# Kernel optimization log

Hardware: AMD Instinct MI355X
Metric: run time of the kernel (lower is better)

## Reference

```python
import jax, jax.numpy as jnp
import numpy as np

N_HEAD = 16
N_KV = 4
ROT = 128  # rotary_dim == head_dim
BASE = 10000
N_CTX = 1024


def make_sincos(n_ctx, rotary_dim, base):
    # GPT-NeoX style (rotary_adjacent_pairs=False): freq repeated twice
    pos = jnp.arange(n_ctx, dtype=jnp.float32)
    dim = jnp.arange(rotary_dim // 2, dtype=jnp.float32)
    freq = jnp.float32(base) ** (dim / (rotary_dim / 2))
    freq = jnp.tile(freq, 2)  # [rotary_dim]
    angles = pos[:, None] / freq[None, :]  # [n_ctx, rotary_dim]
    return jnp.sin(angles), jnp.cos(angles)


def setup_inputs() -> dict:
    key = jax.random.key(0)
    ks = jax.random.split(key, 5)
    B, T, C = 8, 1024, 2048
    r = N_HEAD // N_KV
    Ckv = C // r
    s = 0.02
    x = jax.random.normal(ks[0], (B, T, C), jnp.float32)
    wq = jax.random.normal(ks[1], (C, C), jnp.float32) * s
    wk = jax.random.normal(ks[2], (C, Ckv), jnp.float32) * s
    wv = jax.random.normal(ks[3], (C, Ckv), jnp.float32) * s
    wo = jax.random.normal(ks[4], (C, C), jnp.float32) * s
    sin, cos = make_sincos(N_CTX, ROT, BASE)
    return dict(x=x, wq=wq, wk=wk, wv=wv, wo=wo, sin=sin, cos=cos)


def _rope(x, sin, cos):
    # x: [B, H, T, hd]; rotary applied to first ROT dims (here ROT == hd)
    T = x.shape[2]
    n = ROT // 2
    x_rot = x[..., :ROT]
    x_pass = x[..., ROT:]
    # rotate_every_two (NeoX style): [x0..x_{n-1}, x_n..] -> [-x_n.., x0..]
    x_flip = jnp.concatenate([-x_rot[..., n:], x_rot[..., :n]], axis=-1)
    c = cos[None, None, :T, :]
    s = sin[None, None, :T, :]
    x_rotated = x_rot * c + x_flip * s
    return jnp.concatenate([x_rotated, x_pass], axis=-1)


def reference(x, wq, wk, wv, wo, sin, cos):
    B, T, C = x.shape
    H = N_HEAD
    hd = C // H
    r = H // N_KV
    q = (x @ wq).reshape(B, T, H, hd).transpose(0, 2, 1, 3)  # [B,H,T,hd]
    # Original: repeat_interleave along seq dim then view(B,T,H,hd).
    # Equivalent to tiling the kv channel vector r times per position.
    k = jnp.tile(x @ wk, (1, 1, r)).reshape(B, T, H, hd).transpose(0, 2, 1, 3)
    v = jnp.tile(x @ wv, (1, 1, r)).reshape(B, T, H, hd).transpose(0, 2, 1, 3)
    q = _rope(q, sin, cos)
    k = _rope(k, sin, cos)
    att = jnp.einsum('bhqd,bhkd->bhqk', q, k) / jnp.sqrt(jnp.float32(hd))
    causal = jnp.tril(jnp.ones((T, T), dtype=bool))
    att = jnp.where(causal[None, None], att, -jnp.inf)
    att = jax.nn.softmax(att, axis=-1)
    y = jnp.einsum('bhqk,bhkd->bhqd', att, v)
    y = y.transpose(0, 2, 1, 3).reshape(B, T, C)
    return y @ wo
```

## Files before the change

kernel.cpp:

```cpp
#include <hip/hip_runtime.h>

typedef __attribute__((ext_vector_type(8))) short short8;
typedef __attribute__((ext_vector_type(4))) float f32x4;

#define B_    8
#define T_    1024
#define C_    2048
#define H_    16
#define HKV_  4
#define HD_   128
#define M_    8192
#define NQKV_ 3072
#define KDIM_ 2048

__device__ __forceinline__ unsigned short f2bf(float f) {
  unsigned u = __float_as_uint(f);
  u += 0x7FFF + ((u >> 16) & 1);
  return (unsigned short)(u >> 16);
}
__device__ __forceinline__ float bf2f(unsigned short h) {
  return __uint_as_float(((unsigned)h) << 16);
}

__device__ __forceinline__ void async16(const unsigned short* g, unsigned short* l) {
  __builtin_amdgcn_global_load_lds(
      (const unsigned int __attribute__((address_space(1)))*)g,
      (unsigned int __attribute__((address_space(3)))*)l,
      16, 0, 0);
}

__global__ __launch_bounds__(256) void cvt_bf16_kernel(const float* __restrict__ in,
                                                       unsigned short* __restrict__ out) {
  int idx = blockIdx.x * 256 + threadIdx.x;
  float4 v = ((const float4*)in)[idx];
  ushort4 o;
  o.x = f2bf(v.x); o.y = f2bf(v.y); o.z = f2bf(v.z); o.w = f2bf(v.w);
  ((ushort4*)out)[idx] = o;
}

__global__ __launch_bounds__(256) void tpose_f32_bf16(const float* __restrict__ in,
                                                      unsigned short* __restrict__ out,
                                                      int Cc, int ldo) {
  __shared__ unsigned short tile[32][33];
  int c0 = blockIdx.x * 32, r0 = blockIdx.y * 32;
  int tx = threadIdx.x, ty = threadIdx.y;
#pragma unroll
  for (int j = 0; j < 4; j++)
    tile[ty + j * 8][tx] = f2bf(in[(size_t)(r0 + ty + j * 8) * Cc + c0 + tx]);
  __syncthreads();
#pragma unroll
  for (int j = 0; j < 4; j++)
    out[(size_t)(c0 + ty + j * 8) * ldo + r0 + tx] = tile[tx][ty + j * 8];
}

__global__ __launch_bounds__(256) void vtpose(const unsigned short* __restrict__ qkv,
                                              unsigned short* __restrict__ vt) {
  __shared__ unsigned short tile[32][33];
  int b = blockIdx.z;
  int c0 = blockIdx.x * 32, t0 = blockIdx.y * 32;
  int tx = threadIdx.x, ty = threadIdx.y;
  const unsigned short* src = qkv + (size_t)b * T_ * NQKV_ + 2560;
#pragma unroll
  for (int j = 0; j < 4; j++)
    tile[ty + j * 8][tx] = src[(size_t)(t0 + ty + j * 8) * NQKV_ + c0 + tx];
  __syncthreads();
  unsigned short* dst = vt + (size_t)b * 512 * T_;
#pragma unroll
  for (int j = 0; j < 4; j++)
    dst[(size_t)(c0 + ty + j * 8) * T_ + t0 + tx] = tile[tx][ty + j * 8];
}

__global__ __launch_bounds__(256) void rope_kernel(const unsigned short* __restrict__ qkv,
                                                   const float* __restrict__ sinp,
                                                   const float* __restrict__ cosp,
                                                   unsigned short* __restrict__ qatt,
                                                   unsigned short* __restrict__ katt) {
  int m = blockIdx.x;
  int b = m >> 10, t = m & 1023;
  int tid = threadIdx.x;
  int d = tid & 63;
  const unsigned short* row = qkv + (size_t)m * NQKV_;
  float c0 = cosp[t * 128 + d], s0 = sinp[t * 128 + d];
  float c1 = cosp[t * 128 + d + 64], s1 = sinp[t * 128 + d + 64];
#pragma unroll
  for (int h0 = 0; h0 < 16; h0 += 4) {
    int h = h0 + (tid >> 6);
    float x0 = bf2f(row[h * 128 + d]);
    float x1 = bf2f(row[h * 128 + d + 64]);
    size_t o = ((size_t)(b * 16 + h) * 1024 + t) * 128 + d;
    qatt[o]      = f2bf(x0 * c0 - x1 * s0);
    qatt[o + 64] = f2bf(x1 * c1 + x0 * s1);
  }
  {
    int kh = tid >> 6;
    float x0 = bf2f(row[2048 + kh * 128 + d]);
    float x1 = bf2f(row[2048 + kh * 128 + d + 64]);
    size_t o = ((size_t)(b * 4 + kh) * 1024 + t) * 128 + d;
    katt[o]      = f2bf(x0 * c0 - x1 * s0);
    katt[o + 64] = f2bf(x1 * c1 + x0 * s1);
  }
}

template <int OUTF32>
__global__ __launch_bounds__(256) void gemm_bf16(const unsigned short* __restrict__ A,
                                                 const unsigned short* __restrict__ BT,
                                                 void* __restrict__ Cout, int N) {
  __shared__ unsigned short lA[128 * 32];
  __shared__ unsigned short lB[128 * 32];
  const int K = KDIM_;
  int tid = threadIdx.x;
  int lane = tid & 63;
  int w = tid >> 6;
  int quad = lane >> 4, l16 = lane & 15;
  int bm = blockIdx.y, bn = blockIdx.x;
  const unsigned short* Ab = A + (size_t)bm * 128 * K;
  const unsigned short* Bb = BT + (size_t)bn * 128 * K;
  int i0 = tid, i1 = tid + 256;
  int ra0 = i0 >> 2, ca0 = (i0 & 3) * 8;
  int ra1 = i1 >> 2, ca1 = (i1 & 3) * 8;
  int wm = (w >> 1) * 64, wn = (w & 1) * 64;
  f32x4 acc[4][4] = {};
  for (int k0 = 0; k0 < K; k0 += 32) {
    __syncthreads();
    async16(Ab + (size_t)ra0 * K + k0 + ca0, &lA[i0 * 8]);
    async16(Ab + (size_t)ra1 * K + k0 + ca1, &lA[i1 * 8]);
    async16(Bb + (size_t)ra0 * K + k0 + ca0, &lB[i0 * 8]);
    async16(Bb + (size_t)ra1 * K + k0 + ca1, &lB[i1 * 8]);
    __syncthreads();
    short8 af[4], bfr[4];
#pragma unroll
    for (int mt = 0; mt < 4; mt++)
      af[mt] = *(const short8*)&lA[(wm + mt * 16 + l16) * 32 + quad * 8];
#pragma unroll
    for (int nt = 0; nt < 4; nt++)
      bfr[nt] = *(const short8*)&lB[(wn + nt * 16 + l16) * 32 + quad * 8];
#pragma unroll
    for (int mt = 0; mt < 4; mt++)
#pragma unroll
      for (int nt = 0; nt < 4; nt++)
        acc[mt][nt] = __builtin_amdgcn_mfma_f32_16x16x32_bf16(af[mt], bfr[nt], acc[mt][nt], 0, 0, 0);
  }
#pragma unroll
  for (int mt = 0; mt < 4; mt++) {
#pragma unroll
    for (int nt = 0; nt < 4; nt++) {
      int n = bn * 128 + wn + nt * 16 + l16;
#pragma unroll
      for (int r = 0; r < 4; r++) {
        int m = bm * 128 + wm + mt * 16 + quad * 4 + r;
        if (OUTF32)
          ((float*)Cout)[(size_t)m * N + n] = acc[mt][nt][r];
        else
          ((unsigned short*)Cout)[(size_t)m * N + n] = f2bf(acc[mt][nt][r]);
      }
    }
  }
}

__global__ __launch_bounds__(256, 2) void attn_kernel(const unsigned short* __restrict__ Q,
                                                      const unsigned short* __restrict__ Km,
                                                      const unsigned short* __restrict__ Vt,
                                                      unsigned short* __restrict__ Y) {
  __shared__ __align__(16) unsigned short lK[2][8192];
  __shared__ __align__(16) unsigned short lV[2][8192];
  __shared__ __align__(16) unsigned short lP[4608];
  int tid = threadIdx.x;
  int lane = tid & 63, w = tid >> 6;
  int quad = lane >> 4, l16 = lane & 15;
  int pq = blockIdx.x;
  int bh = blockIdx.y;
  int b = bh >> 4, h = bh & 15, kh = h & 3;
  const unsigned short* Kb = Km + (size_t)(b * 4 + kh) * T_ * 128;
  const unsigned short* Vb = Vt + (size_t)(b * 4 + kh) * 128 * T_;
  const float sc = 0.12751744690989f;
  unsigned short* pb = &lP[w * 1152];
  const int sw = (l16 & 3) * 8;

  int krow[4], kcol[4], vrow[4], vcol[4];
#pragma unroll
  for (int j = 0; j < 4; j++) {
    int i = tid + j * 256;
    int tq = (i & 3) ^ ((i >> 2) & 3);
    krow[j] = (i >> 2) & 63;
    kcol[j] = (i >> 8) * 32 + tq * 8;
    vrow[j] = (i >> 2) & 127;
    vcol[j] = (i >> 9) * 32 + tq * 8;
  }

  for (int ph = 0; ph < 2; ph++) {
    int qt = ph ? pq : 7 - pq;
    int qrow0 = qt * 128 + w * 32;
    const unsigned short* Qb = Q + ((size_t)bh * T_ + qrow0) * 128;
    short8 qf[2][4];
#pragma unroll
    for (int mt = 0; mt < 2; mt++)
#pragma unroll
      for (int ks = 0; ks < 4; ks++)
        qf[mt][ks] = *(const short8*)&Qb[(mt * 16 + l16) * 128 + ks * 32 + quad * 8];
    f32x4 o[2][8] = {};
    float m_r[2][4], l_r[2][4];
#pragma unroll
    for (int mt = 0; mt < 2; mt++)
#pragma unroll
      for (int r = 0; r < 4; r++) {
        m_r[mt][r] = -1e30f;
        l_r[mt][r] = 0.f;
      }
    int ntile = 2 * qt + 2;

    if (ph) __syncthreads();
#pragma unroll
    for (int j = 0; j < 4; j++)
      async16(Kb + (size_t)krow[j] * 128 + kcol[j], &lK[0][(tid + j * 256) * 8]);
#pragma unroll
    for (int j = 0; j < 4; j++)
      async16(Vb + (size_t)vrow[j] * T_ + vcol[j], &lV[0][(tid + j * 256) * 8]);
    asm volatile("s_waitcnt vmcnt(0)" ::: "memory");
    __syncthreads();

    int cur = 0;
    for (int kt = 0; kt < ntile; kt++) {
      int n0 = kt * 64;
      if (kt + 1 < ntile) {
        int n1 = n0 + 64;
#pragma unroll
        for (int j = 0; j < 4; j++)
          async16(Kb + (size_t)(n1 + krow[j]) * 128 + kcol[j], &lK[cur ^ 1][(tid + j * 256) * 8]);
#pragma unroll
        for (int j = 0; j < 4; j++)
          async16(Vb + (size_t)vrow[j] * T_ + n1 + vcol[j], &lV[cur ^ 1][(tid + j * 256) * 8]);
      }
      const unsigned short* lKc = lK[cur];
      const unsigned short* lVc = lV[cur];
      f32x4 s[2][4] = {};
      __builtin_amdgcn_s_setprio(1);
#pragma unroll
      for (int ct = 0; ct < 4; ct++) {
        short8 kf[4];
#pragma unroll
        for (int ks = 0; ks < 4; ks++)
          kf[ks] = *(const short8*)&lKc[ks * 2048 + (ct * 16 + l16) * 32 + (quad * 8 ^ sw)];
#pragma unroll
        for (int ks = 0; ks < 4; ks++) {
          s[0][ct] = __builtin_amdgcn_mfma_f32_16x16x32_bf16(qf[0][ks], kf[ks], s[0][ct], 0, 0, 0);
          s[1][ct] = __builtin_amdgcn_mfma_f32_16x16x32_bf16(qf[1][ks], kf[ks], s[1][ct], 0, 0, 0);
        }
      }
      __builtin_amdgcn_s_setprio(0);
      if (kt >= 2 * qt) {
#pragma unroll
        for (int mt = 0; mt < 2; mt++)
#pragma unroll
          for (int ct = 0; ct < 4; ct++) {
            int n = n0 + ct * 16 + l16;
#pragma unroll
            for (int r = 0; r < 4; r++) {
              int q = qrow0 + mt * 16 + quad * 4 + r;
              if (n > q) s[mt][ct][r] = -1e30f;
            }
          }
      }
      float alpha[2][4], msc[2][4];
#pragma unroll
      for (int mt = 0; mt < 2; mt++)
#pragma unroll
        for (int r = 0; r < 4; r++) {
          float v = fmaxf(fmaxf(s[mt][0][r], s[mt][1][r]), fmaxf(s[mt][2][r], s[mt][3][r]));
#pragma unroll
          for (int off = 1; off < 16; off <<= 1)
            v = fmaxf(v, __shfl_xor(v, off));
          float mn = fmaxf(m_r[mt][r], v);
          alpha[mt][r] = exp2f((m_r[mt][r] - mn) * sc);
          m_r[mt][r] = mn;
          msc[mt][r] = mn * sc;
        }
#pragma unroll
      for (int mt = 0; mt < 2; mt++)
#pragma unroll
        for (int ct = 0; ct < 4; ct++)
#pragma unroll
          for (int r = 0; r < 4; r++)
            s[mt][ct][r] = exp2f(fmaf(s[mt][ct][r], sc, -msc[mt][r]));
#pragma unroll
      for (int ct = 0; ct < 4; ct++)
#pragma unroll
        for (int r = 0; r < 4; r++)
          pb[(quad * 4 + r) * 72 + ct * 16 + l16] = f2bf(s[0][ct][r]);
#pragma unroll
      for (int mt = 0; mt < 2; mt++)
#pragma unroll
        for (int r = 0; r < 4; r++)
          l_r[mt][r] = l_r[mt][r] * alpha[mt][r] +
                       (s[mt][0][r] + s[mt][1][r]) + (s[mt][2][r] + s[mt][3][r]);
      bool needr = false;
#pragma unroll
      for (int mt = 0; mt < 2; mt++)
#pragma unroll
        for (int r = 0; r < 4; r++)
          needr |= (alpha[mt][r] != 1.0f);
      if (__any(needr)) {
#pragma unroll
        for (int mt = 0; mt < 2; mt++)
#pragma unroll
          for (int dt = 0; dt < 8; dt++)
#pragma unroll
            for (int r = 0; r < 4; r++)
              o[mt][dt][r] *= alpha[mt][r];
      }
      __builtin_amdgcn_s_waitcnt(0xC07F);
      short8 pa0[2];
#pragma unroll
      for (int ks2 = 0; ks2 < 2; ks2++)
        pa0[ks2] = *(const short8*)&pb[l16 * 72 + ks2 * 32 + quad * 8];
      __builtin_amdgcn_s_waitcnt(0xC07F);
      asm volatile("" ::: "memory");
#pragma unroll
      for (int ct = 0; ct < 4; ct++)
#pragma unroll
        for (int r = 0; r < 4; r++)
          pb[(quad * 4 + r) * 72 + ct * 16 + l16] = f2bf(s[1][ct][r]);
      __builtin_amdgcn_s_waitcnt(0xC07F);
      short8 pa1[2];
#pragma unroll
      for (int ks2 = 0; ks2 < 2; ks2++)
        pa1[ks2] = *(const short8*)&pb[l16 * 72 + ks2 * 32 + quad * 8];
      __builtin_amdgcn_s_setprio(1);
#pragma unroll
      for (int dt = 0; dt < 8; dt++) {
#pragma unroll
        for (int ks2 = 0; ks2 < 2; ks2++) {
          short8 vf = *(const short8*)&lVc[ks2 * 4096 + (dt * 16 + l16) * 32 + (quad * 8 ^ sw)];
          o[0][dt] = __builtin_amdgcn_mfma_f32_16x16x32_bf16(pa0[ks2], vf, o[0][dt], 0, 0, 0);
          o[1][dt] = __builtin_amdgcn_mfma_f32_16x16x32_bf16(pa1[ks2], vf, o[1][dt], 0, 0, 0);
        }
      }
      __builtin_amdgcn_s_setprio(0);
      if (kt + 1 < ntile) {
        asm volatile("s_waitcnt vmcnt(0)" ::: "memory");
        __syncthreads();
        cur ^= 1;
      }
    }
#pragma unroll
    for (int mt = 0; mt < 2; mt++)
#pragma unroll
      for (int r = 0; r < 4; r++) {
        float v = l_r[mt][r];
#pragma unroll
        for (int off = 1; off < 16; off <<= 1)
          v += __shfl_xor(v, off);
        l_r[mt][r] = v;
      }
#pragma unroll
    for (int mt = 0; mt < 2; mt++)
#pragma unroll
      for (int r = 0; r < 4; r++) {
        int q = qrow0 + mt * 16 + quad * 4 + r;
        float inv = 1.f / l_r[mt][r];
        size_t base = ((size_t)(b * 1024 + q)) * 2048 + h * 128 + l16;
#pragma unroll
        for (int dt = 0; dt < 8; dt++)
          Y[base + dt * 16] = f2bf(o[mt][dt][r] * inv);
      }
  }
}

extern "C" void kernel_launch(void* const* d_in, const int* in_sizes, int n_in,
                              void* d_out, int out_size, void* d_ws, size_t ws_size,
                              hipStream_t stream) {
  const float* x    = (const float*)d_in[0];
  const float* wq   = (const float*)d_in[1];
  const float* wk   = (const float*)d_in[2];
  const float* wv   = (const float*)d_in[3];
  const float* wo   = (const float*)d_in[4];
  const float* sinp = (const float*)d_in[5];
  const float* cosp = (const float*)d_in[6];

  char* ws = (char*)d_ws;
  unsigned short* WCATT = (unsigned short*)(ws);
  unsigned short* WOT   = (unsigned short*)(ws + 12582912);
  unsigned short* XBF   = (unsigned short*)(ws + 20971520);
  unsigned short* QKV   = (unsigned short*)(ws + 54525952);
  unsigned short* KATT  = (unsigned short*)(ws + 104857600);
  unsigned short* VT    = (unsigned short*)(ws + 113246208);
  unsigned short* QATT  = XBF;
  unsigned short* Y     = QKV;

  dim3 tb(32, 8);
  cvt_bf16_kernel<<<16384, 256, 0, stream>>>(x, XBF);
  tpose_f32_bf16<<<dim3(64, 64), tb, 0, stream>>>(wq, WCATT, 2048, 2048);
  tpose_f32_bf16<<<dim3(16, 64), tb, 0, stream>>>(wk, WCATT + (size_t)2048 * 2048, 512, 2048);
  tpose_f32_bf16<<<dim3(16, 64), tb, 0, stream>>>(wv, WCATT + (size_t)2560 * 2048, 512, 2048);
  tpose_f32_bf16<<<dim3(64, 64), tb, 0, stream>>>(wo, WOT, 2048, 2048);
  gemm_bf16<0><<<dim3(24, 64), 256, 0, stream>>>(XBF, WCATT, QKV, 3072);
  rope_kernel<<<8192, 256, 0, stream>>>(QKV, sinp, cosp, QATT, KATT);
  vtpose<<<dim3(16, 32, 8), tb, 0, stream>>>(QKV, VT);
  attn_kernel<<<dim3(4, 128), 256, 0, stream>>>(QATT, KATT, VT, Y);
  gemm_bf16<1><<<dim3(16, 64), 256, 0, stream>>>(Y, WOT, d_out, 2048);
}
```

Baseline: 478.5 us.

## Rewrite GEMM with double-buffered LDS, larger tiles, swizzle and block remapping

Replaces the single-buffered 128x128x32 GEMM with a 256x128x64 tile on 512 threads. Global-to-LDS copies are double-buffered so the next K slab loads while MFMAs run on the current one. LDS columns are XOR-swizzled to cut bank conflicts, and workgroups are remapped in an XCD-aware order for L2 reuse. It also adds setprio around the MFMA bursts, at the cost of more LDS (96KB per block) and more complex synchronisation.

```diff
diff --git a/kernel.cpp b/kernel.cpp
--- a/kernel.cpp
+++ b/kernel.cpp
@@ -102,52 +102,117 @@
 }
 
 template <int OUTF32>
-__global__ __launch_bounds__(256) void gemm_bf16(const unsigned short* __restrict__ A,
-                                                 const unsigned short* __restrict__ BT,
-                                                 void* __restrict__ Cout, int N) {
-  __shared__ unsigned short lA[128 * 32];
-  __shared__ unsigned short lB[128 * 32];
+__global__ __launch_bounds__(512, 2) void gemm_v2(const unsigned short* __restrict__ A,
+                                                  const unsigned short* __restrict__ BT,
+                                                  void* __restrict__ Cout, int N) {
+  __shared__ __align__(16) unsigned short lA[2][256 * 64];
+  __shared__ __align__(16) unsigned short lB[2][128 * 64];
   const int K = KDIM_;
   int tid = threadIdx.x;
   int lane = tid & 63;
   int w = tid >> 6;
   int quad = lane >> 4, l16 = lane & 15;
-  int bm = blockIdx.y, bn = blockIdx.x;
-  const unsigned short* Ab = A + (size_t)bm * 128 * K;
+  int wm = w >> 1, wn = w & 1;
+  int gx = gridDim.x;
+  int nwg = gx * gridDim.y;
+  int lin = blockIdx.y * gx + blockIdx.x;
+  int cpx = nwg >> 3;
+  int swz = (lin & 7) * cpx + (lin >> 3);
+  int bm = swz / gx, bn = swz % gx;
+  const unsigned short* Ab = A + (size_t)bm * 256 * K;
   const unsigned short* Bb = BT + (size_t)bn * 128 * K;
-  int i0 = tid, i1 = tid + 256;
-  int ra0 = i0 >> 2, ca0 = (i0 & 3) * 8;
-  int ra1 = i1 >> 2, ca1 = (i1 & 3) * 8;
-  int wm = (w >> 1) * 64, wn = (w & 1) * 64;
+  int klin = (tid & 7) * 8;
+  int arow[4], acol[4];
+#pragma unroll
+  for (int j = 0; j < 4; j++) {
+    int r = (j * 512 + tid) >> 3;
+    arow[j] = r;
+    acol[j] = klin ^ (((r >> 2) & 3) * 16);
+  }
+  int brow[2], bcol[2];
+#pragma unroll
+  for (int j = 0; j < 2; j++) {
+    int r = (j * 512 + tid) >> 3;
+    brow[j] = r;
+    bcol[j] = klin ^ (((r >> 2) & 3) * 16);
+  }
+  const int rsw = ((l16 >> 2) & 3) * 16;
   f32x4 acc[4][4] = {};
-  for (int k0 = 0; k0 < K; k0 += 32) {
-    __syncthreads();
-    async16(Ab + (size_t)ra0 * K + k0 + ca0, &lA[i0 * 8]);
-    async16(Ab + (size_t)ra1 * K + k0 + ca1, &lA[i1 * 8]);
-    async16(Bb + (size_t)ra0 * K + k0 + ca0, &lB[i0 * 8]);
-    async16(Bb + (size_t)ra1 * K + k0 + ca1, &lB[i1 * 8]);
-    __syncthreads();
-    short8 af[4], bfr[4];
-#pragma unroll
-    for (int mt = 0; mt < 4; mt++)
-      af[mt] = *(const short8*)&lA[(wm + mt * 16 + l16) * 32 + quad * 8];
+#pragma unroll
+  for (int j = 0; j < 4; j++)
+    async16(Ab + (size_t)arow[j] * K + acol[j], &lA[0][(j * 512 + tid) * 8]);
+#pragma unroll
+  for (int j = 0; j < 2; j++)
+    async16(Bb + (size_t)brow[j] * K + bcol[j], &lB[0][(j * 512 + tid) * 8]);
+  asm volatile("s_waitcnt vmcnt(0)" ::: "memory");
+  __builtin_amdgcn_s_barrier();
+  int cur = 0;
+  for (int kt = 0; kt < 32; kt++) {
+    const unsigned short* pA = lA[cur];
+    const unsigned short* pB = lB[cur];
+    short8 af[2][2], bfr[4][2];
+#pragma unroll
+    for (int mt = 0; mt < 2; mt++)
+#pragma unroll
+      for (int ks = 0; ks < 2; ks++)
+        af[mt][ks] = *(const short8*)&pA[(wm * 64 + mt * 16 + l16) * 64 +
+                                         ((ks * 32 + quad * 8) ^ rsw)];
 #pragma unroll
     for (int nt = 0; nt < 4; nt++)
-      bfr[nt] = *(const short8*)&lB[(wn + nt * 16 + l16) * 32 + quad * 8];
-#pragma unroll
-    for (int mt = 0; mt < 4; mt++)
+#pragma unroll
+      for (int ks = 0; ks < 2; ks++)
+        bfr[nt][ks] = *(const short8*)&pB[(wn * 64 + nt * 16 + l16) * 64 +
+                                          ((ks * 32 + quad * 8) ^ rsw)];
+    if (kt < 31) {
+      int k0 = (kt + 1) * 64;
+#pragma unroll
+      for (int j = 0; j < 4; j++)
+        async16(Ab + (size_t)arow[j] * K + k0 + acol[j], &lA[cur ^ 1][(j * 512 + tid) * 8]);
+#pragma unroll
+      for (int j = 0; j < 2; j++)
+        async16(Bb + (size_t)brow[j] * K + k0 + bcol[j], &lB[cur ^ 1][(j * 512 + tid) * 8]);
+    }
+    __builtin_amdgcn_s_barrier();
+    __builtin_amdgcn_s_setprio(1);
+#pragma unroll
+    for (int mt = 0; mt < 2; mt++)
 #pragma unroll
       for (int nt = 0; nt < 4; nt++)
-        acc[mt][nt] = __builtin_amdgcn_mfma_f32_16x16x32_bf16(af[mt], bfr[nt], acc[mt][nt], 0, 0, 0);
+#pragma unroll
+        for (int ks = 0; ks < 2; ks++)
+          acc[mt][nt] = __builtin_amdgcn_mfma_f32_16x16x32_bf16(af[mt][ks], bfr[nt][ks],
+                                                                acc[mt][nt], 0, 0, 0);
+    __builtin_amdgcn_s_setprio(0);
+    __builtin_amdgcn_s_barrier();
+    short8 ag[2][2];
+#pragma unroll
+    for (int mt = 0; mt < 2; mt++)
+#pragma unroll
+      for (int ks = 0; ks < 2; ks++)
+        ag[mt][ks] = *(const short8*)&pA[(wm * 64 + (mt + 2) * 16 + l16) * 64 +
+                                         ((ks * 32 + quad * 8) ^ rsw)];
+    __builtin_amdgcn_s_setprio(1);
+#pragma unroll
+    for (int mt = 0; mt < 2; mt++)
+#pragma unroll
+      for (int nt = 0; nt < 4; nt++)
+#pragma unroll
+        for (int ks = 0; ks < 2; ks++)
+          acc[mt + 2][nt] = __builtin_amdgcn_mfma_f32_16x16x32_bf16(ag[mt][ks], bfr[nt][ks],
+                                                                    acc[mt + 2][nt], 0, 0, 0);
+    __builtin_amdgcn_s_setprio(0);
+    asm volatile("s_waitcnt vmcnt(0)" ::: "memory");
+    __builtin_amdgcn_s_barrier();
+    cur ^= 1;
   }
 #pragma unroll
   for (int mt = 0; mt < 4; mt++) {
 #pragma unroll
     for (int nt = 0; nt < 4; nt++) {
-      int n = bn * 128 + wn + nt * 16 + l16;
+      int n = bn * 128 + wn * 64 + nt * 16 + l16;
 #pragma unroll
       for (int r = 0; r < 4; r++) {
-        int m = bm * 128 + wm + mt * 16 + quad * 4 + r;
+        int m = bm * 256 + wm * 64 + mt * 16 + quad * 4 + r;
         if (OUTF32)
           ((float*)Cout)[(size_t)m * N + n] = acc[mt][nt][r];
         else
@@ -392,9 +457,9 @@
   tpose_f32_bf16<<<dim3(16, 64), tb, 0, stream>>>(wk, WCATT + (size_t)2048 * 2048, 512, 2048);
   tpose_f32_bf16<<<dim3(16, 64), tb, 0, stream>>>(wv, WCATT + (size_t)2560 * 2048, 512, 2048);
   tpose_f32_bf16<<<dim3(64, 64), tb, 0, stream>>>(wo, WOT, 2048, 2048);
-  gemm_bf16<0><<<dim3(24, 64), 256, 0, stream>>>(XBF, WCATT, QKV, 3072);
+  gemm_v2<0><<<dim3(24, 32), 512, 0, stream>>>(XBF, WCATT, QKV, 3072);
   rope_kernel<<<8192, 256, 0, stream>>>(QKV, sinp, cosp, QATT, KATT);
   vtpose<<<dim3(16, 32, 8), tb, 0, stream>>>(QKV, VT);
   attn_kernel<<<dim3(4, 128), 256, 0, stream>>>(QATT, KATT, VT, Y);
-  gemm_bf16<1><<<dim3(16, 64), 256, 0, stream>>>(Y, WOT, d_out, 2048);
-}
+  gemm_v2<1><<<dim3(16, 32), 512, 0, stream>>>(Y, WOT, d_out, 2048);
+}
```

Result: faster. 466.7 us (-2.4%).
